# Optimization experiments

Hardware: AMD Instinct MI355X
Metric: run time of the kernel (lower is better)

Reference implementation:

```python
import jax, jax.numpy as jnp
import numpy as np

DIM = 192
HEADS = 4
CTX = 256
HID = int(DIM * 2.66)  # 510


def _dwconv(x, w):
    # x: (b,c,h,w), w: (c,1,3,3) depthwise
    return jax.lax.conv_general_dilated(
        x, w, window_strides=(1, 1), padding='SAME',
        dimension_numbers=('NCHW', 'OIHW', 'NCHW'),
        feature_group_count=x.shape[1])


def _conv1x1(x, w):
    # w: (out, in)
    return jnp.einsum('oc,bchw->bohw', w, x)


def _layernorm(x, weight, bias):
    # WithBias LayerNorm over channel dim (last dim after to_3d == channels)
    mu = x.mean(axis=1, keepdims=True)
    var = ((x - mu) ** 2).mean(axis=1, keepdims=True)
    xn = (x - mu) / jnp.sqrt(var + 1e-5)
    return xn * weight[None, :, None, None] + bias[None, :, None, None]


def setup_inputs() -> dict:
    key = jax.random.key(0)
    ks = jax.random.split(key, 16)
    s = 0.02
    inp = {
        'x': jax.random.normal(ks[0], (8, DIM, 128, 128), jnp.float32),
        'context_emb': jax.random.normal(ks[1], (8, CTX), jnp.float32),
        'ln1_w': jnp.ones((DIM,), jnp.float32),
        'ln1_b': jnp.zeros((DIM,), jnp.float32),
        'ln2_w': jnp.ones((DIM,), jnp.float32),
        'ln2_b': jnp.zeros((DIM,), jnp.float32),
        'w_qkv': jax.random.normal(ks[2], (3 * DIM, DIM), jnp.float32) * s,
        'w_qkv_dw': jax.random.normal(ks[3], (3 * DIM, 1, 3, 3), jnp.float32) * s,
        'w_proj': jax.random.normal(ks[4], (DIM, DIM), jnp.float32) * s,
        'base_temp': jnp.ones((HEADS, 1, 1), jnp.float32),
        'ta_w1': jax.random.normal(ks[5], (DIM // 4, CTX), jnp.float32) * s,
        'ta_b1': jnp.zeros((DIM // 4,), jnp.float32),
        'ta_w2': jax.random.normal(ks[6], (HEADS, DIM // 4), jnp.float32) * s,
        'ta_b2': jnp.zeros((HEADS,), jnp.float32),
        'vg_w': jax.random.normal(ks[7], (DIM, CTX), jnp.float32) * s,
        'vg_b': jnp.zeros((DIM,), jnp.float32),
        'w_local': jax.random.normal(ks[8], (DIM, 1, 3, 3), jnp.float32) * s,
        'w_ffn_in': jax.random.normal(ks[9], (2 * HID, DIM), jnp.float32) * s,
        'w_ffn_dw': jax.random.normal(ks[10], (2 * HID, 1, 3, 3), jnp.float32) * s,
        'w_ffn_out': jax.random.normal(ks[11], (DIM, HID), jnp.float32) * s,
    }
    return inp


def _forward(x, context_emb, ln1_w, ln1_b, ln2_w, ln2_b, w_qkv, w_qkv_dw,
             w_proj, base_temp, ta_w1, ta_b1, ta_w2, ta_b2, vg_w, vg_b,
             w_local, w_ffn_in, w_ffn_dw, w_ffn_out):
    b, c, h, w = x.shape
    hd = c // HEADS
    scale = hd ** (-0.5)

    # ---- Attention branch ----
    residual = x
    xn = _layernorm(x, ln1_w, ln1_b)

    # context adapters
    t = jax.nn.relu(context_emb @ ta_w1.T + ta_b1) @ ta_w2.T + ta_b2  # (b,heads)
    temp_factor = jax.nn.sigmoid(t)[:, :, None, None] * 2.0 + 0.5    # (b,heads,1,1)
    total_temp = base_temp[None] * temp_factor
    v_gate = jax.nn.sigmoid(context_emb @ vg_w.T + vg_b)             # (b,dim)
    v_gate = v_gate.reshape(b, HEADS, hd, 1)

    qkv = _dwconv(_conv1x1(xn, w_qkv), w_qkv_dw)
    q, k, v = jnp.split(qkv, 3, axis=1)

    def heads_flat(t4):
        return t4.reshape(b, HEADS, hd, h * w)

    qf = heads_flat(q)
    kf = heads_flat(k)
    vf = heads_flat(v)
    qf = qf / jnp.maximum(jnp.linalg.norm(qf, axis=-1, keepdims=True), 1e-12)
    kf = kf / jnp.maximum(jnp.linalg.norm(kf, axis=-1, keepdims=True), 1e-12)

    attn = jnp.einsum('bhcn,bhdn->bhcd', qf, kf) * scale  # (b,heads,hd,hd)
    attn = jax.nn.softmax(attn * total_temp, axis=-1)

    out_global = jnp.einsum('bhcd,bhdn->bhcn', attn, vf * v_gate)
    out_global = out_global.reshape(b, c, h, w)
    out_local = _dwconv(v, w_local)
    x = residual + _conv1x1(out_global + out_local, w_proj)

    # ---- GDFN branch ----
    residual = x
    xn = _layernorm(x, ln2_w, ln2_b)
    y = _dwconv(_conv1x1(xn, w_ffn_in), w_ffn_dw)
    y1, y2 = jnp.split(y, 2, axis=1)
    y = jax.nn.gelu(y1, approximate=False) * y2
    x = residual + _conv1x1(y, w_ffn_out)
    return x


def reference(x, context_emb, ln1_w, ln1_b, ln2_w, ln2_b, w_qkv, w_qkv_dw,
              w_proj, base_temp, ta_w1, ta_b1, ta_w2, ta_b2, vg_w, vg_b,
              w_local, w_ffn_in, w_ffn_dw, w_ffn_out):
    return _forward(x, context_emb, ln1_w, ln1_b, ln2_w, ln2_b, w_qkv,
                    w_qkv_dw, w_proj, base_temp, ta_w1, ta_b1, ta_w2, ta_b2,
                    vg_w, vg_b, w_local, w_ffn_in, w_ffn_dw, w_ffn_out)
```

## Files before the change

### kernel.cpp

```cpp
#include <hip/hip_runtime.h>
#include <math.h>

#define NB 8
#define NC 192
#define NH 128
#define NW 128
#define HW 16384
#define NQ 576
#define NHID 510
#define NHIDP 512
#define NG2 1020
#define NG2P 1024

#define BROWS 32
#define BSLOTS 34
#define BPIX (BSLOTS * NW)
#define BIPIX (BROWS * NW)

typedef unsigned short u16;
typedef short s16x8 __attribute__((ext_vector_type(8)));
typedef float f32x4 __attribute__((ext_vector_type(4)));

#define MFMA_BF16(a, b, c) __builtin_amdgcn_mfma_f32_16x16x32_bf16((a), (b), (c), 0, 0, 0)

__device__ __forceinline__ u16 f2bf(float f) {
  union { float f; unsigned u; } v; v.f = f;
  unsigned r = v.u + 0x7fffu + ((v.u >> 16) & 1u);
  return (u16)(r >> 16);
}
__device__ __forceinline__ float bf2f(u16 h) {
  union { unsigned u; float f; } v; v.u = ((unsigned)h) << 16; return v.f;
}
__device__ __forceinline__ float lo2f(unsigned u) {
  union { unsigned u; float f; } v; v.u = u << 16; return v.f;
}
__device__ __forceinline__ float hi2f(unsigned u) {
  union { unsigned u; float f; } v; v.u = u & 0xffff0000u; return v.f;
}
__device__ __forceinline__ unsigned pack2(float a, float b) {
  return (unsigned)f2bf(a) | ((unsigned)f2bf(b) << 16);
}
__device__ __forceinline__ int xcdswz(int bid, int nwg) {
  return (bid & 7) * (nwg >> 3) + (bid >> 3);
}

__device__ __forceinline__ void gll16(const void* g, void* l) {
  __builtin_amdgcn_global_load_lds(
      (const __attribute__((address_space(1))) void*)g,
      (__attribute__((address_space(3))) void*)l, 16, 0, 0);
}

__global__ void k_prep(const float* __restrict__ wq, const float* __restrict__ wfi,
                       const float* __restrict__ wfo,
                       u16* __restrict__ oq, u16* __restrict__ ofi, u16* __restrict__ ofo) {
  const int n1 = NQ * NC, n2 = NG2P * NC, n3 = NC * NHIDP;
  for (int i = blockIdx.x * blockDim.x + threadIdx.x; i < n1 + n2 + n3;
       i += gridDim.x * blockDim.x) {
    if (i < n1) {
      int row = i / NC, col = i - row * NC;
      int g = col >> 3, o = col & 7;
      int sc = (((g ^ (row & 7)) << 3) | o);
      oq[i] = f2bf(wq[row * NC + sc]);
    } else if (i < n1 + n2) {
      int j = i - n1; int row = j / NC, col = j - row * NC;
      int g = col >> 3, o = col & 7;
      int sc = (((g ^ (row & 7)) << 3) | o);
      u16 v = 0;
      if (row < NG2) v = f2bf(wfi[row * NC + sc]);
      ofi[j] = v;
    } else {
      int j = i - n1 - n2; int row = j >> 9, col = j & 511;
      u16 v = 0;
      if (col < NHID) v = f2bf(wfo[row * NHID + col]);
      ofo[j] = v;
    }
  }
}

__global__ void k_ctx(const float* __restrict__ ce, const float* __restrict__ taw1,
                      const float* __restrict__ tab1, const float* __restrict__ taw2,
                      const float* __restrict__ tab2, const float* __restrict__ vgw,
                      const float* __restrict__ vgb, const float* __restrict__ btemp,
                      float* __restrict__ tempt, float* __restrict__ vg) {
  int b = blockIdx.x, t = threadIdx.x;
  __shared__ float sce[256];
  __shared__ float shid[48];
  sce[t] = ce[b * 256 + t];
  __syncthreads();
  if (t < 48) {
    float s = tab1[t];
    for (int j = 0; j < 256; j++) s = fmaf(taw1[t * 256 + j], sce[j], s);
    shid[t] = fmaxf(s, 0.f);
  }
  __syncthreads();
  if (t < 4) {
    float s = tab2[t];
    for (int j = 0; j < 48; j++) s = fmaf(taw2[t * 48 + j], shid[j], s);
    float sg = 1.f / (1.f + expf(-s));
    tempt[b * 4 + t] = btemp[t] * (sg * 2.f + 0.5f);
  }
  if (t < 192) {
    float s = vgb[t];
    for (int j = 0; j < 256; j++) s = fmaf(vgw[t * 256 + j], sce[j], s);
    vg[b * 192 + t] = 1.f / (1.f + expf(-s));
  }
}

__global__ __launch_bounds__(256, 2)
void k_ln_gemm_band(const float* __restrict__ in, const unsigned* __restrict__ res,
                    const float* __restrict__ lnw,
                    const float* __restrict__ lnb, const u16* __restrict__ wbf,
                    u16* __restrict__ out, int nchunks, int row_start, int slot0) {
  __shared__ u16 Xn[64 * 200];
  __shared__ u16 Wc[2][64 * 192];
  __shared__ float red[512];
  __shared__ float stats[128];
  int t = threadIdx.x;
  int lane = t & 63, wv = t >> 6;
  int bpb = gridDim.x >> 3;
  int nb = xcdswz(blockIdx.x, gridDim.x);
  int b = nb / bpb;
  int rb = nb - b * bpb;
  int gpx0 = row_start * NW + rb * 64;
  int opx0 = slot0 * NW + rb * 64;
  const float* xp = in + (size_t)b * NC * HW + gpx0 + lane;
  const unsigned* rp = res + (size_t)b * 96 * HW + gpx0 + lane;
  bool hasres = (res != nullptr);
  float vals[48];
  float s = 0.f, s2 = 0.f;
#pragma unroll
  for (int j = 0; j < 48; j += 2) {
    float v0 = xp[(size_t)(wv * 48 + j) * HW];
    float v1 = xp[(size_t)(wv * 48 + j + 1) * HW];
    if (hasres) {
      unsigned pr = rp[(size_t)(wv * 24 + (j >> 1)) * HW];
      v0 += lo2f(pr); v1 += hi2f(pr);
    }
    vals[j] = v0; vals[j + 1] = v1;
    s += v0 + v1; s2 = fmaf(v0, v0, s2); s2 = fmaf(v1, v1, s2);
  }
  red[wv * 64 + lane] = s;
  red[256 + wv * 64 + lane] = s2;
  __syncthreads();
  if (t < 64) {
    float m = 0.f, q = 0.f;
#pragma unroll
    for (int k = 0; k < 4; k++) { m += red[k * 64 + t]; q += red[256 + k * 64 + t]; }
    m *= (1.f / 192.f);
    float var = q * (1.f / 192.f) - m * m;
    stats[t] = m; stats[64 + t] = rsqrtf(var + 1e-5f);
  }
  __syncthreads();
  float mu = stats[lane], rs = stats[64 + lane];
#pragma unroll
  for (int j = 0; j < 48; j += 2) {
    int c = wv * 48 + j;
    float xa = (vals[j] - mu) * rs * lnw[c] + lnb[c];
    float xb = (vals[j + 1] - mu) * rs * lnw[c + 1] + lnb[c + 1];
    *(unsigned*)&Xn[lane * 200 + c] = pack2(xa, xb);
  }
  int r = lane & 15, grp = lane >> 4;
  int key = r & 7;
  int ostride = nchunks << 6;

  auto stageW = [&](int nc, int buf) {
    const u16* src = wbf + (size_t)nc * 64 * 192;
    for (int i = t; i < 1536; i += 256)
      gll16(&src[i * 8], &Wc[buf][i * 8]);
  };

  stageW(0, 0);
  __syncthreads();
  int cur = 0;
  for (int nc = 0; nc < nchunks; nc++) {
    if (nc + 1 < nchunks) stageW(nc + 1, cur ^ 1);
    f32x4 z = {0.f, 0.f, 0.f, 0.f};
    f32x4 acc0 = z, acc1 = z, acc2 = z, acc3 = z;
#pragma unroll
    for (int ks = 0; ks < 6; ks++) {
      int k0 = ks * 32 + grp * 8;
      int gsw = ((((ks << 2) + grp) ^ key) << 3);
      s16x8 a = *(s16x8*)&Xn[(wv * 16 + r) * 200 + k0];
      acc0 = MFMA_BF16(a, *(s16x8*)&Wc[cur][r * 192 + gsw], acc0);
      acc1 = MFMA_BF16(a, *(s16x8*)&Wc[cur][(16 + r) * 192 + gsw], acc1);
      acc2 = MFMA_BF16(a, *(s16x8*)&Wc[cur][(32 + r) * 192 + gsw], acc2);
      acc3 = MFMA_BF16(a, *(s16x8*)&Wc[cur][(48 + r) * 192 + gsw], acc3);
    }
    u16* op = out + ((size_t)b * BPIX + opx0 + wv * 16 + grp * 4) * ostride + nc * 64 + r;
#pragma unroll
    for (int i = 0; i < 4; i++) {
      op[(size_t)i * ostride] = f2bf(acc0[i]);
      op[(size_t)i * ostride + 16] = f2bf(acc1[i]);
      op[(size_t)i * ostride + 32] = f2bf(acc2[i]);
      op[(size_t)i * ostride + 48] = f2bf(acc3[i]);
    }
    __syncthreads();
    cur ^= 1;
  }
}

__global__ __launch_bounds__(256, 4)
void k_dw_attn_band(const u16* __restrict__ qb_band, const float* __restrict__ wdw,
                    u16* __restrict__ qkb, u16* __restrict__ vpm,
                    float* __restrict__ ssq, int r0, const u16* __restrict__ zp) {
  __shared__ u16 Hl[6 * 18 * 64];
  __shared__ float sred[8 * 64];
  int t = threadIdx.x;
  int nb = xcdswz(blockIdx.x, gridDim.x);
  int cc = nb % 9;
  int rem = nb / 9;
  int b = rem >> 6; int r2 = rem & 63;
  int h0l = (r2 >> 3) * 4, w0 = (r2 & 7) * 16;
  int c0 = cc * 64;
  const s16x8 z8 = {0, 0, 0, 0, 0, 0, 0, 0};
  for (int i = t; i < 864; i += 256) {
    int px = i >> 3, sg = i & 7;
    int hh = px / 18, ww = px % 18;
    int slot = h0l + hh;
    int gh = r0 - 1 + slot;
    int gw = w0 - 1 + ww;
    const void* g = (gh >= 0 && gh < NH && gw >= 0 && gw < NW)
        ? (const void*)&qb_band[((size_t)b * BPIX + slot * NW + gw) * NQ + c0 + sg * 8]
        : (const void*)zp;
    gll16(g, &Hl[i * 8]);
  }
  __syncthreads();
  int cp = t & 31, psub = t >> 5;
  int pr = psub >> 1, pc0 = (psub & 1) * 8;
  int gc = c0 + 2 * cp;
  float wg0[9], wg1[9];
#pragma unroll
  for (int q = 0; q < 9; q++) { wg0[q] = wdw[gc * 9 + q]; wg1[q] = wdw[(gc + 1) * 9 + q]; }
  bool isv = (c0 >= 384);
  float sq0 = 0.f, sq1 = 0.f;
  s16x8 ov0 = z8, ov1 = z8;
#pragma unroll
  for (int j = 0; j < 8; j++) {
    int pc = pc0 + j;
    float a0 = 0.f, a1 = 0.f;
#pragma unroll
    for (int dr = 0; dr < 3; dr++)
#pragma unroll
      for (int dc = 0; dc < 3; dc++) {
        unsigned u = *(const unsigned*)&Hl[((pr + dr) * 18 + pc + dc) * 64 + 2 * cp];
        a0 = fmaf(lo2f(u), wg0[dr * 3 + dc], a0);
        a1 = fmaf(hi2f(u), wg1[dr * 3 + dc], a1);
      }
    u16 u0 = f2bf(a0), u1 = f2bf(a1);
    if (isv) {
      int gp = (r0 + h0l + pr) * NW + w0 + pc;
      *(unsigned*)&vpm[((size_t)b * HW + gp) * 192 + (gc - 384)] =
          (unsigned)u0 | ((unsigned)u1 << 16);
    } else {
      ov0[j] = (short)u0; ov1[j] = (short)u1;
      float f0 = bf2f(u0), f1 = bf2f(u1);
      sq0 = fmaf(f0, f0, sq0); sq1 = fmaf(f1, f1, sq1);
    }
  }
  if (!isv) {
    int lpx = (h0l + pr) * NW + w0 + pc0;
    *(s16x8*)&qkb[((size_t)b * 384 + gc) * BIPIX + lpx] = ov0;
    *(s16x8*)&qkb[((size_t)b * 384 + gc + 1) * BIPIX + lpx] = ov1;
    sred[psub * 64 + 2 * cp] = sq0;
    sred[psub * 64 + 2 * cp + 1] = sq1;
    __syncthreads();
    if (t < 64) {
      float sa = 0.f;
#pragma unroll
      for (int p8 = 0; p8 < 8; p8++) sa += sred[p8 * 64 + t];
      atomicAdd(&ssq[b * 384 + c0 + t], sa);
    }
  }
}

__global__ __launch_bounds__(256, 2)
void k_attn_band(const u16* __restrict__ qkb, float* __restrict__ attn) {
  __shared__ float par[4 * 2304];
  int t = threadIdx.x;
  int lane = t & 63, wv = t >> 6;
  int r = lane & 15, grp = lane >> 4;
  int nb = xcdswz(blockIdx.x, gridDim.x);
  int bh = nb >> 3, kc = nb & 7;
  int b = bh >> 2, h = bh & 3;
  const u16* qb = qkb + ((size_t)b * 384 + h * 48) * BIPIX;
  const u16* kb = qkb + ((size_t)b * 384 + 192 + h * 48) * BIPIX;
  f32x4 z = {0.f, 0.f, 0.f, 0.f};
  f32x4 acc[3][3];
#pragma unroll
  for (int i = 0; i < 3; i++)
#pragma unroll
    for (int j = 0; j < 3; j++) acc[i][j] = z;
  int kbase = kc * 512 + wv * 128 + grp * 8;
#pragma unroll
  for (int ks = 0; ks < 4; ks++) {
    int k0 = kbase + ks * 32;
    s16x8 af[3], bf[3];
#pragma unroll
    for (int mt = 0; mt < 3; mt++) af[mt] = *(const s16x8*)&qb[(size_t)(mt * 16 + r) * BIPIX + k0];
#pragma unroll
    for (int nt = 0; nt < 3; nt++) bf[nt] = *(const s16x8*)&kb[(size_t)(nt * 16 + r) * BIPIX + k0];
#pragma unroll
    for (int mt = 0; mt < 3; mt++)
#pragma unroll
      for (int nt = 0; nt < 3; nt++) acc[mt][nt] = MFMA_BF16(af[mt], bf[nt], acc[mt][nt]);
  }
#pragma unroll
  for (int mt = 0; mt < 3; mt++)
#pragma unroll
    for (int nt = 0; nt < 3; nt++)
#pragma unroll
      for (int i = 0; i < 4; i++)
        par[wv * 2304 + (mt * 16 + grp * 4 + i) * 48 + nt * 16 + r] = acc[mt][nt][i];
  __syncthreads();
  float* ag = attn + (size_t)bh * 2304;
  for (int i = t; i < 2304; i += 256)
    atomicAdd(&ag[i], par[i] + par[2304 + i] + par[4608 + i] + par[6912 + i]);
}

__global__ void k_softmax(float* __restrict__ attn, const float* __restrict__ ssq,
                          const float* __restrict__ tempt, const float* __restrict__ vg) {
  int bh = blockIdx.x, b = bh >> 2, h = bh & 3;
  int t = threadIdx.x;
  __shared__ float srk[48], svg[48];
  if (t < 48) {
    float nk = sqrtf(ssq[b * 384 + 192 + h * 48 + t]);
    srk[t] = 1.f / fmaxf(nk, 1e-12f);
    svg[t] = vg[b * 192 + h * 48 + t];
  }
  __syncthreads();
  if (t < 48) {
    float nq = sqrtf(ssq[b * 384 + h * 48 + t]);
    float rq = 1.f / fmaxf(nq, 1e-12f);
    float sc = 0.14433756729740643f * tempt[b * 4 + h] * rq;
    float* row = attn + (size_t)bh * 2304 + t * 48;
    float l[48]; float mx = -1e30f;
#pragma unroll
    for (int d = 0; d < 48; d++) { l[d] = row[d] * srk[d] * sc; mx = fmaxf(mx, l[d]); }
    float ss = 0.f;
#pragma unroll
    for (int d = 0; d < 48; d++) { l[d] = expf(l[d] - mx); ss += l[d]; }
    float inv = 1.f / ss;
#pragma unroll
    for (int d = 0; d < 48; d++) row[d] = l[d] * inv * svg[d];
  }
}

__global__ __launch_bounds__(256)
void k_wd(const float* __restrict__ attn, const float* __restrict__ wp,
          u16* __restrict__ wdg) {
  __shared__ float am[4 * 48 * 48];
  int b = blockIdx.x >> 3, oc = blockIdx.x & 7;
  int t = threadIdx.x;
  const float* ag = attn + (size_t)b * 4 * 2304;
  for (int i = t; i < 9216; i += 256) am[i] = ag[i];
  __syncthreads();
  u16* wdb = wdg + (size_t)b * 192 * 384;
  for (int idx = t; idx < 24 * 384; idx += 256) {
    int oo = idx / 384, j = idx % 384;
    int o = oc * 24 + oo;
    float val;
    if (j < 192) {
      int hj = j / 48, dj = j % 48;
      const float* wpo = wp + o * 192 + hj * 48;
      const float* ap = am + hj * 2304 + dj;
      float sa = 0.f;
#pragma unroll
      for (int c = 0; c < 48; c++) sa = fmaf(wpo[c], ap[c * 48], sa);
      val = sa;
    } else {
      val = wp[o * 192 + (j - 192)];
    }
    wdb[o * 384 + j] = f2bf(val);
  }
}

__global__ __launch_bounds__(256, 2)
void k_proj(const u16* __restrict__ vpm, const float* __restrict__ wl,
            const u16* __restrict__ wdg, unsigned* __restrict__ proj,
            const u16* __restrict__ zp) {
  __shared__ u16 Hl[2][6 * 18 * 64];
  __shared__ u16 Xl[64 * 392];
  int t = threadIdx.x;
  int nb = xcdswz(blockIdx.x, gridDim.x);
  int b = nb >> 8; int r2 = nb & 255;
  int h0 = (r2 >> 3) * 4, w0 = (r2 & 7) * 16;
  int cp = t & 31, psub = t >> 5;
  int pr = psub >> 1, pc0 = (psub & 1) * 8;
  int lane = t & 63, wv = t >> 6;
  int r = lane & 15, grp = lane >> 4;

  auto stageH = [&](int c3s, int buf) {
    int c0s = c3s * 64;
    for (int i = t; i < 864; i += 256) {
      int px = i >> 3, sg = i & 7;
      int hh = px / 18, ww = px % 18;
      int gh = h0 - 1 + hh, gw = w0 - 1 + ww;
      const void* g = (gh >= 0 && gh < NH && gw >= 0 && gw < NW)
          ? (const void*)&vpm[((size_t)b * HW + gh * NW + gw) * 192 + c0s + sg * 8]
          : (const void*)zp;
      gll16(g, &Hl[buf][i * 8]);
    }
  };

  stageH(0, 0);
  __syncthreads();
  int cur = 0;
  for (int c3 = 0; c3 < 3; c3++) {
    if (c3 < 2) stageH(c3 + 1, cur ^ 1);
    int c0 = c3 * 64;
    int gc = c0 + 2 * cp;
    float wg0[9], wg1[9];
#pragma unroll
    for (int q = 0; q < 9; q++) { wg0[q] = wl[gc * 9 + q]; wg1[q] = wl[(gc + 1) * 9 + q]; }
#pragma unroll
    for (int j = 0; j < 8; j++) {
      int pc = pc0 + j; int p = pr * 16 + pc;
      float a0 = 0.f, a1 = 0.f; unsigned uc = 0;
#pragma unroll
      for (int dr = 0; dr < 3; dr++)
#pragma unroll
        for (int dc = 0; dc < 3; dc++) {
          unsigned u = *(const unsigned*)&Hl[cur][((pr + dr) * 18 + pc + dc) * 64 + 2 * cp];
          if (dr == 1 && dc == 1) uc = u;
          a0 = fmaf(lo2f(u), wg0[dr * 3 + dc], a0);
          a1 = fmaf(hi2f(u), wg1[dr * 3 + dc], a1);
        }
      *(unsigned*)&Xl[p * 392 + gc] = uc;
      *(unsigned*)&Xl[p * 392 + 192 + gc] = pack2(a0, a1);
    }
    __syncthreads();
    cur ^= 1;
  }
  const u16* wdb = wdg + (size_t)b * 192 * 384;
  f32x4 z = {0.f, 0.f, 0.f, 0.f};
  f32x4 acc[3][4];
#pragma unroll
  for (int i = 0; i < 3; i++)
#pragma unroll
    for (int j = 0; j < 4; j++) acc[i][j] = z;
#pragma unroll 2
  for (int ks = 0; ks < 12; ks++) {
    int k0 = ks * 32 + grp * 8;
    s16x8 b0 = *(s16x8*)&Xl[r * 392 + k0];
    s16x8 b1 = *(s16x8*)&Xl[(16 + r) * 392 + k0];
    s16x8 b2 = *(s16x8*)&Xl[(32 + r) * 392 + k0];
    s16x8 b3 = *(s16x8*)&Xl[(48 + r) * 392 + k0];
#pragma unroll
    for (int mt = 0; mt < 3; mt++) {
      s16x8 a = *(const s16x8*)&wdb[(size_t)(wv * 48 + mt * 16 + r) * 384 + k0];
      acc[mt][0] = MFMA_BF16(a, b0, acc[mt][0]);
      acc[mt][1] = MFMA_BF16(a, b1, acc[mt][1]);
      acc[mt][2] = MFMA_BF16(a, b2, acc[mt][2]);
      acc[mt][3] = MFMA_BF16(a, b3, acc[mt][3]);
    }
  }
#pragma unroll
  for (int mt = 0; mt < 3; mt++)
#pragma unroll
    for (int nt = 0; nt < 4; nt++) {
      int cpair = wv * 24 + mt * 8 + grp * 2;
      size_t pb = ((size_t)b * 96 + cpair) * HW + (h0 + nt) * NW + w0 + r;
      proj[pb] = pack2(acc[mt][nt][0], acc[mt][nt][1]);
      proj[pb + HW] = pack2(acc[mt][nt][2], acc[mt][nt][3]);
    }
}

__global__ __launch_bounds__(256, 2)
void k_gelu_ffn_band(const u16* __restrict__ ypre, const float* __restrict__ wdwf,
                     const u16* __restrict__ wfo, const float* __restrict__ x,
                     const unsigned* __restrict__ proj,
                     float* __restrict__ out, int r0, const u16* __restrict__ zp) {
  __shared__ u16 H1[2][6 * 18 * 64];
  __shared__ u16 H2[2][6 * 18 * 72];
  __shared__ u16 Yc[64 * 80];
  int t = threadIdx.x;
  int nb = xcdswz(blockIdx.x, gridDim.x);
  int b = nb >> 6; int r2 = nb & 63;
  int h0l = (r2 >> 3) * 4, w0 = (r2 & 7) * 16;
  int cp = t & 31, psub = t >> 5;
  int pr = psub >> 1, pc0 = (psub & 1) * 8;
  int lane = t & 63, wv = t >> 6;
  int r = lane & 15, grp = lane >> 4;
  int jl = 2 * cp;

  auto stage = [&](int jc, int buf) {
    int j0s = jc * 64;
    int base2 = j0s + 504;
    for (int i = t; i < 864; i += 256) {
      int px = i >> 3, sg = i & 7;
      int hh = px / 18, ww = px % 18;
      int slot = h0l + hh;
      int gh = r0 - 1 + slot, gw = w0 - 1 + ww;
      const void* g = (gh >= 0 && gh < NH && gw >= 0 && gw < NW)
          ? (const void*)&ypre[((size_t)b * BPIX + slot * NW + gw) * NG2P + j0s + sg * 8]
          : (const void*)zp;
      gll16(g, &H1[buf][i * 8]);
    }
    for (int i = t; i < 972; i += 256) {
      int px = i / 9, sg = i - px * 9;
      int hh = px / 18, ww = px % 18;
      int slot = h0l + hh;
      int gh = r0 - 1 + slot, gw = w0 - 1 + ww;
      const void* g = (gh >= 0 && gh < NH && gw >= 0 && gw < NW)
          ? (const void*)&ypre[((size_t)b * BPIX + slot * NW + gw) * NG2P + base2 + sg * 8]
          : (const void*)zp;
      gll16(g, &H2[buf][i * 8]);
    }
  };

  f32x4 z = {0.f, 0.f, 0.f, 0.f};
  f32x4 acc[3][4];
#pragma unroll
  for (int i = 0; i < 3; i++)
#pragma unroll
    for (int j = 0; j < 4; j++) acc[i][j] = z;

  stage(0, 0);
  __syncthreads();
  int cur = 0;
  for (int jc = 0; jc < 8; jc++) {
    if (jc < 7) stage(jc + 1, cur ^ 1);
    int j0 = jc * 64;
    int j = j0 + jl;
    bool v0 = (j < NHID), v1 = (j + 1 < NHID);
    float w1a[9], w1b[9], w2a[9], w2b[9];
#pragma unroll
    for (int q = 0; q < 9; q++) {
      w1a[q] = 0.f; w1b[q] = 0.f; w2a[q] = 0.f; w2b[q] = 0.f;
      if (v0) { w1a[q] = wdwf[j * 9 + q]; w2a[q] = wdwf[(j + NHID) * 9 + q]; }
      if (v1) { w1b[q] = wdwf[(j + 1) * 9 + q]; w2b[q] = wdwf[(j + 1 + NHID) * 9 + q]; }
    }
#pragma unroll
    for (int jj = 0; jj < 8; jj++) {
      int pc = pc0 + jj;
      float d1a = 0.f, d1b = 0.f, d2a = 0.f, d2b = 0.f;
#pragma unroll
      for (int dr = 0; dr < 3; dr++)
#pragma unroll
        for (int dc = 0; dc < 3; dc++) {
          int q = dr * 3 + dc;
          unsigned u1 = *(const unsigned*)&H1[cur][((pr + dr) * 18 + pc + dc) * 64 + jl];
          unsigned u2 = *(const unsigned*)&H2[cur][((pr + dr) * 18 + pc + dc) * 72 + jl + 6];
          d1a = fmaf(lo2f(u1), w1a[q], d1a); d1b = fmaf(hi2f(u1), w1b[q], d1b);
          d2a = fmaf(lo2f(u2), w2a[q], d2a); d2b = fmaf(hi2f(u2), w2b[q], d2b);
        }
      float ga = 0.5f * d1a * (1.f + erff(d1a * 0.70710678118654752f));
      float gb = 0.5f * d1b * (1.f + erff(d1b * 0.70710678118654752f));
      float ya = v0 ? ga * d2a : 0.f;
      float yb = v1 ? gb * d2b : 0.f;
      int lp = pr * 16 + pc;
      *(unsigned*)&Yc[lp * 80 + jl] = pack2(ya, yb);
    }
    __syncthreads();
#pragma unroll
    for (int ks = 0; ks < 2; ks++) {
      int k0 = ks * 32 + grp * 8;
      s16x8 b0 = *(s16x8*)&Yc[r * 80 + k0];
      s16x8 b1 = *(s16x8*)&Yc[(16 + r) * 80 + k0];
      s16x8 b2 = *(s16x8*)&Yc[(32 + r) * 80 + k0];
      s16x8 b3 = *(s16x8*)&Yc[(48 + r) * 80 + k0];
#pragma unroll
      for (int mt = 0; mt < 3; mt++) {
        s16x8 a = *(const s16x8*)&wfo[(size_t)(wv * 48 + mt * 16 + r) * NHIDP + j0 + k0];
        acc[mt][0] = MFMA_BF16(a, b0, acc[mt][0]);
        acc[mt][1] = MFMA_BF16(a, b1, acc[mt][1]);
        acc[mt][2] = MFMA_BF16(a, b2, acc[mt][2]);
        acc[mt][3] = MFMA_BF16(a, b3, acc[mt][3]);
      }
    }
    __syncthreads();
    cur ^= 1;
  }
#pragma unroll
  for (int mt = 0; mt < 3; mt++)
#pragma unroll
    for (int nt = 0; nt < 4; nt++) {
      size_t base = ((size_t)b * NC + wv * 48 + mt * 16 + grp * 4) * HW +
                    (r0 + h0l + nt) * NW + w0 + r;
      int cpair = wv * 24 + mt * 8 + grp * 2;
      size_t pb = ((size_t)b * 96 + cpair) * HW + (r0 + h0l + nt) * NW + w0 + r;
      unsigned p0 = proj[pb], p1 = proj[pb + HW];
      out[base] = acc[mt][nt][0] + x[base] + lo2f(p0);
      out[base + HW] = acc[mt][nt][1] + x[base + HW] + hi2f(p0);
      out[base + 2 * (size_t)HW] = acc[mt][nt][2] + x[base + 2 * (size_t)HW] + lo2f(p1);
      out[base + 3 * (size_t)HW] = acc[mt][nt][3] + x[base + 3 * (size_t)HW] + hi2f(p1);
    }
}

extern "C" void kernel_launch(void* const* d_in, const int* in_sizes, int n_in,
                              void* d_out, int out_size, void* d_ws, size_t ws_size,
                              hipStream_t stream) {
  const float* x      = (const float*)d_in[0];
  const float* ce     = (const float*)d_in[1];
  const float* ln1w   = (const float*)d_in[2];
  const float* ln1b   = (const float*)d_in[3];
  const float* ln2w   = (const float*)d_in[4];
  const float* ln2b   = (const float*)d_in[5];
  const float* wqkv   = (const float*)d_in[6];
  const float* wqkvdw = (const float*)d_in[7];
  const float* wproj  = (const float*)d_in[8];
  const float* btemp  = (const float*)d_in[9];
  const float* taw1   = (const float*)d_in[10];
  const float* tab1   = (const float*)d_in[11];
  const float* taw2   = (const float*)d_in[12];
  const float* tab2   = (const float*)d_in[13];
  const float* vgw    = (const float*)d_in[14];
  const float* vgb    = (const float*)d_in[15];
  const float* wlocal = (const float*)d_in[16];
  const float* wffni  = (const float*)d_in[17];
  const float* wffndw = (const float*)d_in[18];
  const float* wffno  = (const float*)d_in[19];
  float* outp = (float*)d_out;
  char* ws = (char*)d_ws;

  const size_t REQUIRED = 174270848ULL;
  if (ws_size < REQUIRED) {
    hipMemsetAsync(d_out, 0, (size_t)out_size * 4, stream);
    return;
  }
  u16*   wq_bf   = (u16*)(ws + 0);
  u16*   wfi_bf  = (u16*)(ws + 221184);
  u16*   wfo_bf  = (u16*)(ws + 614400);
  float* tempt   = (float*)(ws + 811008);
  float* vg      = (float*)(ws + 811136);
  float* ssq     = (float*)(ws + 817280);
  float* attn    = (float*)(ws + 829568);
  u16*   wdg     = (u16*)(ws + 1124480);
  u16*   qkvband = (u16*)(ws + 2304128);
  u16*   qkband  = (u16*)(ws + 42412160);
  u16*   ypreband= (u16*)(ws + 2304128);
  u16*   vpm     = (u16*)(ws + 73607296);
  unsigned* proj = (unsigned*)(ws + 123938944);
  u16*   zp      = (u16*)(ws + 174270592);

  hipMemsetAsync(ws + 817280, 0, 12288 + 294912, stream);
  hipMemsetAsync(ws + 174270592, 0, 256, stream);
  k_prep<<<512, 256, 0, stream>>>(wqkv, wffni, wffno, wq_bf, wfi_bf, wfo_bf);
  k_ctx<<<8, 256, 0, stream>>>(ce, taw1, tab1, taw2, tab2, vgw, vgb, btemp, tempt, vg);

  for (int band = 0; band < 4; band++) {
    int r0 = band * BROWS;
    int rs = (r0 > 0) ? r0 - 1 : 0;
    int re = (r0 + BROWS + 1 < NH) ? r0 + BROWS + 1 : NH;
    int nr = re - rs;
    int s0 = rs - (r0 - 1);
    k_ln_gemm_band<<<8 * nr * 2, 256, 0, stream>>>(x, nullptr, ln1w, ln1b, wq_bf,
                                                   qkvband, 9, rs, s0);
    k_dw_attn_band<<<9 * 8 * 64, 256, 0, stream>>>(qkvband, wqkvdw, qkband, vpm, ssq, r0, zp);
    k_attn_band<<<32 * 8, 256, 0, stream>>>(qkband, attn);
  }
  k_softmax<<<32, 64, 0, stream>>>(attn, ssq, tempt, vg);
  k_wd<<<64, 256, 0, stream>>>(attn, wproj, wdg);
  k_proj<<<2048, 256, 0, stream>>>(vpm, wlocal, wdg, proj, zp);

  for (int band = 0; band < 4; band++) {
    int r0 = band * BROWS;
    int rs = (r0 > 0) ? r0 - 1 : 0;
    int re = (r0 + BROWS + 1 < NH) ? r0 + BROWS + 1 : NH;
    int nr = re - rs;
    int s0 = rs - (r0 - 1);
    k_ln_gemm_band<<<8 * nr * 2, 256, 0, stream>>>(x, proj, ln2w, ln2b, wfi_bf,
                                                   ypreband, 16, rs, s0);
    k_gelu_ffn_band<<<8 * 64, 256, 0, stream>>>(ypreband, wffndw, wfo_bf, x, proj,
                                                outp, r0, zp);
  }
}
```

Before: 1.096 ms.

## Split FFN-in GEMM across output chunks, halve attn blocks, drop XCD swizzle

Adds an nsplit parameter to the LN+GEMM band kernel so the FFN input projection launches twice as many blocks, each computing half the output-channel chunks. The aim is more parallelism and better occupancy, at the cost of recomputing the LayerNorm for every split. The attention-partial kernel now uses 4 K-chunks instead of 8, with each block looping over 8 k-steps, which trades launched blocks for fewer atomic/partial contributions. The XCD-aware block swizzle is removed from every kernel, which may hurt L2 locality across chiplets.

```diff
diff --git a/kernel.cpp b/kernel.cpp
--- a/kernel.cpp
+++ b/kernel.cpp
@@ -39,9 +39,6 @@
 }
 __device__ __forceinline__ unsigned pack2(float a, float b) {
   return (unsigned)f2bf(a) | ((unsigned)f2bf(b) << 16);
-}
-__device__ __forceinline__ int xcdswz(int bid, int nwg) {
-  return (bid & 7) * (nwg >> 3) + (bid >> 3);
 }
 
 __device__ __forceinline__ void gll16(const void* g, void* l) {
@@ -110,7 +107,8 @@
 void k_ln_gemm_band(const float* __restrict__ in, const unsigned* __restrict__ res,
                     const float* __restrict__ lnw,
                     const float* __restrict__ lnb, const u16* __restrict__ wbf,
-                    u16* __restrict__ out, int nchunks, int row_start, int slot0) {
+                    u16* __restrict__ out, int nchunks, int nsplit,
+                    int row_start, int slot0) {
   __shared__ u16 Xn[64 * 200];
   __shared__ u16 Wc[2][64 * 192];
   __shared__ float red[512];
@@ -118,9 +116,12 @@
   int t = threadIdx.x;
   int lane = t & 63, wv = t >> 6;
   int bpb = gridDim.x >> 3;
-  int nb = xcdswz(blockIdx.x, gridDim.x);
-  int b = nb / bpb;
-  int rb = nb - b * bpb;
+  int b = blockIdx.x / bpb;
+  int rem = blockIdx.x - b * bpb;
+  int rb = rem / nsplit;
+  int sp = rem - rb * nsplit;
+  int nch = nchunks / nsplit;
+  int c0ch = sp * nch;
   int gpx0 = row_start * NW + rb * 64;
   int opx0 = slot0 * NW + rb * 64;
   const float* xp = in + (size_t)b * NC * HW + gpx0 + lane;
@@ -169,11 +170,11 @@
       gll16(&src[i * 8], &Wc[buf][i * 8]);
   };
 
-  stageW(0, 0);
+  stageW(c0ch, 0);
   __syncthreads();
   int cur = 0;
-  for (int nc = 0; nc < nchunks; nc++) {
-    if (nc + 1 < nchunks) stageW(nc + 1, cur ^ 1);
+  for (int nc = c0ch; nc < c0ch + nch; nc++) {
+    if (nc + 1 < c0ch + nch) stageW(nc + 1, cur ^ 1);
     f32x4 z = {0.f, 0.f, 0.f, 0.f};
     f32x4 acc0 = z, acc1 = z, acc2 = z, acc3 = z;
 #pragma unroll
@@ -206,9 +207,8 @@
   __shared__ u16 Hl[6 * 18 * 64];
   __shared__ float sred[8 * 64];
   int t = threadIdx.x;
-  int nb = xcdswz(blockIdx.x, gridDim.x);
-  int cc = nb % 9;
-  int rem = nb / 9;
+  int cc = blockIdx.x % 9;
+  int rem = blockIdx.x / 9;
   int b = rem >> 6; int r2 = rem & 63;
   int h0l = (r2 >> 3) * 4, w0 = (r2 & 7) * 16;
   int c0 = cc * 64;
@@ -279,8 +279,7 @@
   int t = threadIdx.x;
   int lane = t & 63, wv = t >> 6;
   int r = lane & 15, grp = lane >> 4;
-  int nb = xcdswz(blockIdx.x, gridDim.x);
-  int bh = nb >> 3, kc = nb & 7;
+  int bh = blockIdx.x >> 2, kc = blockIdx.x & 3;
   int b = bh >> 2, h = bh & 3;
   const u16* qb = qkb + ((size_t)b * 384 + h * 48) * BIPIX;
   const u16* kb = qkb + ((size_t)b * 384 + 192 + h * 48) * BIPIX;
@@ -290,9 +289,9 @@
   for (int i = 0; i < 3; i++)
 #pragma unroll
     for (int j = 0; j < 3; j++) acc[i][j] = z;
-  int kbase = kc * 512 + wv * 128 + grp * 8;
-#pragma unroll
-  for (int ks = 0; ks < 4; ks++) {
+  int kbase = kc * 1024 + wv * 256 + grp * 8;
+#pragma unroll 2
+  for (int ks = 0; ks < 8; ks++) {
     int k0 = kbase + ks * 32;
     s16x8 af[3], bf[3];
 #pragma unroll
@@ -381,8 +380,7 @@
   __shared__ u16 Hl[2][6 * 18 * 64];
   __shared__ u16 Xl[64 * 392];
   int t = threadIdx.x;
-  int nb = xcdswz(blockIdx.x, gridDim.x);
-  int b = nb >> 8; int r2 = nb & 255;
+  int b = blockIdx.x >> 8; int r2 = blockIdx.x & 255;
   int h0 = (r2 >> 3) * 4, w0 = (r2 & 7) * 16;
   int cp = t & 31, psub = t >> 5;
   int pr = psub >> 1, pc0 = (psub & 1) * 8;
@@ -474,8 +472,7 @@
   __shared__ u16 H2[2][6 * 18 * 72];
   __shared__ u16 Yc[64 * 80];
   int t = threadIdx.x;
-  int nb = xcdswz(blockIdx.x, gridDim.x);
-  int b = nb >> 6; int r2 = nb & 63;
+  int b = blockIdx.x >> 6; int r2 = blockIdx.x & 63;
   int h0l = (r2 >> 3) * 4, w0 = (r2 & 7) * 16;
   int cp = t & 31, psub = t >> 5;
   int pr = psub >> 1, pc0 = (psub & 1) * 8;
@@ -645,9 +642,9 @@
     int nr = re - rs;
     int s0 = rs - (r0 - 1);
     k_ln_gemm_band<<<8 * nr * 2, 256, 0, stream>>>(x, nullptr, ln1w, ln1b, wq_bf,
-                                                   qkvband, 9, rs, s0);
+                                                   qkvband, 9, 1, rs, s0);
     k_dw_attn_band<<<9 * 8 * 64, 256, 0, stream>>>(qkvband, wqkvdw, qkband, vpm, ssq, r0, zp);
-    k_attn_band<<<32 * 8, 256, 0, stream>>>(qkband, attn);
+    k_attn_band<<<32 * 4, 256, 0, stream>>>(qkband, attn);
   }
   k_softmax<<<32, 64, 0, stream>>>(attn, ssq, tempt, vg);
   k_wd<<<64, 256, 0, stream>>>(attn, wproj, wdg);
@@ -659,8 +656,8 @@
     int re = (r0 + BROWS + 1 < NH) ? r0 + BROWS + 1 : NH;
     int nr = re - rs;
     int s0 = rs - (r0 - 1);
-    k_ln_gemm_band<<<8 * nr * 2, 256, 0, stream>>>(x, proj, ln2w, ln2b, wfi_bf,
-                                                   ypreband, 16, rs, s0);
+    k_ln_gemm_band<<<8 * nr * 2 * 2, 256, 0, stream>>>(x, proj, ln2w, ln2b, wfi_bf,
+                                                       ypreband, 16, 2, rs, s0);
     k_gelu_ffn_band<<<8 * 64, 256, 0, stream>>>(ypreband, wffndw, wfo_bf, x, proj,
                                                 outp, r0, zp);
   }
```

After: 1.157 ms. +5.5%, slower.
